# Performance work log

Measured on AMD Instinct MI355X. Metric: run time of the kernel, lower is better.

## Reference

```python
import jax, jax.numpy as jnp
import numpy as np
from jax import lax

HEADS = 8
PS = 4  # window size


def setup_inputs() -> dict:
    key = jax.random.key(0)
    k1, k2, k3, k4 = jax.random.split(key, 4)
    b, c, h, w = 8, 256, 128, 128
    x = jax.random.normal(k1, (b, c, h, w), dtype=jnp.float32)
    W_qkv = jax.random.normal(k2, (3 * c, c), dtype=jnp.float32) * 0.05
    W_dw = jax.random.normal(k3, (3 * c, 1, 3, 3), dtype=jnp.float32) * 0.1
    temperature = jnp.ones((HEADS, 1, 1), dtype=jnp.float32)
    W_proj = jax.random.normal(k4, (c, c), dtype=jnp.float32) * 0.05
    return {"x": x, "W_qkv": W_qkv, "W_dw": W_dw, "temperature": temperature, "W_proj": W_proj}


def _l2norm(t, eps=1e-12):
    # matches torch F.normalize(dim=-1): x / max(||x||_2, eps)
    n = jnp.sqrt(jnp.sum(t * t, axis=-1, keepdims=True))
    return t / jnp.maximum(n, eps)


def reference(x, W_qkv, W_dw, temperature, W_proj):
    b, c, h0, w0 = x.shape
    ps, heads = PS, HEADS
    pad_h = (ps - h0 % ps) % ps
    pad_w = (ps - w0 % ps) % ps
    if pad_h or pad_w:
        x = jnp.pad(x, ((0, 0), (0, 0), (0, pad_h), (0, pad_w)))
    H, W = x.shape[2], x.shape[3]
    nh, nw = H // ps, W // ps
    d = c // heads

    # 1x1 conv -> depthwise 3x3 conv (groups = 3c, padding 1)
    qkv = jnp.einsum('oc,bchw->bohw', W_qkv, x)
    qkv = lax.conv_general_dilated(qkv, W_dw, (1, 1), 'SAME',
                                   feature_group_count=3 * c,
                                   dimension_numbers=('NCHW', 'OIHW', 'NCHW'))
    q, k, v = jnp.split(qkv, 3, axis=1)

    def win(t):
        # b (head d) (nh ps) (nw ps) -> b (nh nw) head d (ps ps)
        t = t.reshape(b, heads, d, nh, ps, nw, ps)
        t = t.transpose(0, 3, 5, 1, 2, 4, 6)  # b nh nw head d ps ps
        return t.reshape(b, nh * nw, heads, d, ps * ps)

    q, k, v = win(q), win(k), win(v)
    q = _l2norm(q)
    k = _l2norm(k)

    # channel attention over head-dim d, keys/queries live in the ps*ps window
    attn = jnp.einsum('bnhde,bnhfe->bnhdf', q, k) * temperature  # (b,n,head,d,d)
    attn = jax.nn.softmax(attn, axis=-1)
    out = jnp.einsum('bnhdf,bnhfe->bnhde', attn, v)  # (b,n,head,d,ps*ps)

    # inverse rearrange -> b (head d) H W
    out = out.reshape(b, nh, nw, heads, d, ps, ps)
    out = out.transpose(0, 3, 4, 1, 5, 2, 6).reshape(b, c, H, W)
    out = jnp.einsum('oc,bchw->bohw', W_proj, out)
    if pad_h or pad_w:
        out = out[:, :, :h0, :w0]
    return out
```

## Files before the change

kernel.cpp:

```cpp
#include <hip/hip_runtime.h>
#include <math.h>


#define HW_ (128*128)
#define CHW_ (256*128*128)

typedef __attribute__((ext_vector_type(8))) short short8;
typedef __attribute__((ext_vector_type(4))) short shortv4;
typedef __attribute__((ext_vector_type(4))) float f32x4;

static __device__ __forceinline__ unsigned short f2bf(float f) {
    unsigned int u = __float_as_uint(f);
    unsigned int r = (u + 0x7fffu + ((u >> 16) & 1u)) >> 16;
    return (unsigned short)r;
}
static __device__ __forceinline__ float bf2f(unsigned short u) {
    return __uint_as_float(((unsigned int)u) << 16);
}

__global__ __launch_bounds__(256) void conv_w(
    const float* __restrict__ Wq, const float* __restrict__ Wp,
    unsigned short* __restrict__ out)
{
    int i = blockIdx.x * 256 + threadIdx.x;
    float v = (i < 196608) ? Wq[i] : Wp[i - 196608];
    out[i] = f2bf(v);
}

__global__ __launch_bounds__(256) void gemm_qkv(
    const unsigned short* __restrict__ A,
    const float* __restrict__ x,
    unsigned short* __restrict__ qkv)
{
    __shared__ __align__(16) char smem[16896];
    const int t = threadIdx.x;
    const int lane = t & 63, wid = t >> 6;
    const int m0 = blockIdx.x * 128;
    const int by = blockIdx.y;
    const int nb = by >> 7;
    const int nloc0 = (by & 127) * 128;
    const int wr = wid >> 1, wc = wid & 1;
    const int l15 = lane & 15, l4 = lane >> 4;

    const unsigned short* srcA[2];
    #pragma unroll
    for (int i = 0; i < 2; ++i) {
        int u = i * 256 + t;
        int r = u >> 2, cs = u & 3;
        int c = cs ^ ((r ^ (r >> 2)) & 3);
        srcA[i] = A + (size_t)(m0 + r) * 256 + c * 8;
    }
    int ar[4];
    #pragma unroll
    for (int i = 0; i < 4; ++i) {
        int rm = wr * 64 + i * 16 + l15;
        ar[i] = rm * 4 + (l4 ^ ((rm ^ (rm >> 2)) & 3));
    }

    const int pl  = (t & 31) * 4;
    const int chq = t >> 5;
    const float* xb = x + (size_t)nb * CHW_ + nloc0 + pl;
    char* Bbase = smem + 8192;
    char* bwp = Bbase + chq * 1056 + pl * 8;

    f32x4 acc[4][4];
    #pragma unroll
    for (int i = 0; i < 4; ++i)
        #pragma unroll
        for (int j = 0; j < 4; ++j)
            acc[i][j] = (f32x4){0.f, 0.f, 0.f, 0.f};

    const short8* Ab = (const short8*)smem;

    for (int k0 = 0; k0 < 256; k0 += 32) {
        __syncthreads();
        #pragma unroll
        for (int i = 0; i < 2; ++i)
            __builtin_amdgcn_global_load_lds(
                (const __attribute__((address_space(1))) void*)(srcA[i] + k0),
                (__attribute__((address_space(3))) void*)(smem + i * 4096 + wid * 1024),
                16, 0, 0);
        float4 vx[4];
        #pragma unroll
        for (int j = 0; j < 4; ++j)
            vx[j] = *reinterpret_cast<const float4*>(
                xb + (size_t)(k0 + chq * 4 + j) * HW_);
        short8 w0, w1;
        #pragma unroll
        for (int p = 0; p < 4; ++p) {
            const float* f0 = (const float*)&vx[0];
            const float* f1 = (const float*)&vx[1];
            const float* f2 = (const float*)&vx[2];
            const float* f3 = (const float*)&vx[3];
            short v0 = (short)f2bf(f0[p]);
            short v1 = (short)f2bf(f1[p]);
            short v2 = (short)f2bf(f2[p]);
            short v3 = (short)f2bf(f3[p]);
            if (p < 2) {
                w0[p * 4 + 0] = v0; w0[p * 4 + 1] = v1;
                w0[p * 4 + 2] = v2; w0[p * 4 + 3] = v3;
            } else {
                w1[(p - 2) * 4 + 0] = v0; w1[(p - 2) * 4 + 1] = v1;
                w1[(p - 2) * 4 + 2] = v2; w1[(p - 2) * 4 + 3] = v3;
            }
        }
        *reinterpret_cast<short8*>(bwp)      = w0;
        *reinterpret_cast<short8*>(bwp + 16) = w1;
        __syncthreads();

        short8 af[4], bf[4];
        #pragma unroll
        for (int i = 0; i < 4; ++i) {
            af[i] = Ab[ar[i]];
            int rn = wc * 64 + i * 16 + l15;
            shortv4 lo = *reinterpret_cast<const shortv4*>(
                Bbase + (l4 * 2) * 1056 + rn * 8);
            shortv4 hi = *reinterpret_cast<const shortv4*>(
                Bbase + (l4 * 2 + 1) * 1056 + rn * 8);
            short8 b;
            b[0] = lo.x; b[1] = lo.y; b[2] = lo.z; b[3] = lo.w;
            b[4] = hi.x; b[5] = hi.y; b[6] = hi.z; b[7] = hi.w;
            bf[i] = b;
        }
        #pragma unroll
        for (int am = 0; am < 4; ++am)
            #pragma unroll
            for (int bn = 0; bn < 4; ++bn)
                acc[am][bn] = __builtin_amdgcn_mfma_f32_16x16x32_bf16(
                    af[am], bf[bn], acc[am][bn], 0, 0, 0);
    }

    unsigned short* Co = qkv + (size_t)nb * (768 * (size_t)HW_) + nloc0;
    float* ep = (float*)smem;
    const int rr = t >> 3, c0 = (t & 7) * 16;
    #pragma unroll
    for (int am = 0; am < 4; ++am) {
        __syncthreads();
        #pragma unroll
        for (int q = 0; q < 4; ++q)
            #pragma unroll
            for (int bn = 0; bn < 4; ++bn)
                ep[(wr * 16 + l4 * 4 + q) * 132 + wc * 64 + bn * 16 + l15] =
                    acc[am][bn][q];
        __syncthreads();
        short8 o0, o1;
        #pragma unroll
        for (int j = 0; j < 8; ++j) {
            o0[j] = (short)f2bf(ep[rr * 132 + c0 + j]);
            o1[j] = (short)f2bf(ep[rr * 132 + c0 + 8 + j]);
        }
        int m = m0 + (rr >> 4) * 64 + am * 16 + (rr & 15);
        unsigned short* p = Co + (size_t)m * 16384 + c0;
        *reinterpret_cast<short8*>(p) = o0;
        *reinterpret_cast<short8*>(p + 8) = o1;
    }
}

template<int BF16OUT>
__global__ __launch_bounds__(256) void gemm_bf16(
    const unsigned short* __restrict__ A,
    const unsigned short* __restrict__ Bt,
    void* __restrict__ Cv,
    size_t strideBatch)
{
    __shared__ __align__(16) char smem[16384];

    const int t = threadIdx.x;
    const int lane = t & 63, wid = t >> 6;
    const int m0 = blockIdx.x * 128;
    const int n0 = blockIdx.y * 128;
    const int nb = n0 >> 14, nloc0 = n0 & 16383;
    const int wr = wid >> 1, wc = wid & 1;
    const int l15 = lane & 15, l4 = lane >> 4;

    const unsigned short* srcA[2];
    const unsigned short* srcB[2];
    #pragma unroll
    for (int i = 0; i < 2; ++i) {
        int u = i * 256 + t;
        int r = u >> 2, cs = u & 3;
        int c = cs ^ ((r ^ (r >> 2)) & 3);
        srcA[i] = A  + (size_t)(m0 + r) * 256 + c * 8;
        srcB[i] = Bt + (size_t)(n0 + r) * 256 + c * 8;
    }

    int ar[4], br[4];
    #pragma unroll
    for (int i = 0; i < 4; ++i) {
        int rm = wr * 64 + i * 16 + l15;
        ar[i] = rm * 4 + (l4 ^ ((rm ^ (rm >> 2)) & 3));
        int rn = wc * 64 + i * 16 + l15;
        br[i] = rn * 4 + (l4 ^ ((rn ^ (rn >> 2)) & 3));
    }

    f32x4 acc[4][4];
    #pragma unroll
    for (int i = 0; i < 4; ++i)
        #pragma unroll
        for (int j = 0; j < 4; ++j)
            acc[i][j] = (f32x4){0.f, 0.f, 0.f, 0.f};

    const short8* Ab = (const short8*)smem;
    const short8* Bb = (const short8*)(smem + 8192);

    for (int k0 = 0; k0 < 256; k0 += 32) {
        __syncthreads();
        #pragma unroll
        for (int i = 0; i < 2; ++i) {
            __builtin_amdgcn_global_load_lds(
                (const __attribute__((address_space(1))) void*)(srcA[i] + k0),
                (__attribute__((address_space(3))) void*)(smem + i * 4096 + wid * 1024),
                16, 0, 0);
            __builtin_amdgcn_global_load_lds(
                (const __attribute__((address_space(1))) void*)(srcB[i] + k0),
                (__attribute__((address_space(3))) void*)(smem + 8192 + i * 4096 + wid * 1024),
                16, 0, 0);
        }
        __syncthreads();
        short8 af[4], bf[4];
        #pragma unroll
        for (int i = 0; i < 4; ++i) { af[i] = Ab[ar[i]]; bf[i] = Bb[br[i]]; }
        #pragma unroll
        for (int am = 0; am < 4; ++am)
            #pragma unroll
            for (int bn = 0; bn < 4; ++bn)
                acc[am][bn] = __builtin_amdgcn_mfma_f32_16x16x32_bf16(
                    af[am], bf[bn], acc[am][bn], 0, 0, 0);
    }

    float* Co = (float*)Cv + (size_t)nb * strideBatch + nloc0;
    #pragma unroll
    for (int am = 0; am < 4; ++am)
        #pragma unroll
        for (int q = 0; q < 4; ++q) {
            int m = m0 + wr * 64 + am * 16 + l4 * 4 + q;
            #pragma unroll
            for (int bn = 0; bn < 4; ++bn)
                Co[(size_t)m * 16384 + wc * 64 + bn * 16 + l15] =
                    acc[am][bn][q];
        }
}

__global__ __launch_bounds__(256) void dwconv_win(
    const unsigned short* __restrict__ qkv,
    const float* __restrict__ Wdw,
    unsigned short* __restrict__ dww)
{
    const int t    = threadIdx.x;
    const int lane = t & 63;
    const int iw   = t & 31;
    const int chl  = t >> 5;
    const int wyl  = blockIdx.x;
    const int ch   = blockIdx.y * 8 + chl;
    const int bz   = blockIdx.z;

    float w[9];
    #pragma unroll
    for (int i = 0; i < 9; ++i) w[i] = Wdw[ch * 9 + i];

    float h[6][6];
    const unsigned short* plane = qkv + (size_t)(bz * 768 + ch) * HW_;
    #pragma unroll
    for (int r = 0; r < 6; ++r) {
        int gy = wyl * 4 - 1 + r;
        float c0 = 0.f, c1 = 0.f, c2 = 0.f, c3 = 0.f;
        if (gy >= 0 && gy < 128) {
            ushort4 u = *reinterpret_cast<const ushort4*>(
                plane + (size_t)gy * 128 + iw * 4);
            c0 = bf2f(u.x); c1 = bf2f(u.y); c2 = bf2f(u.z); c3 = bf2f(u.w);
        }
        float lf = __shfl(c3, (lane + 63) & 63);
        float rt = __shfl(c0, (lane + 1) & 63);
        h[r][0] = (iw == 0)  ? 0.f : lf;
        h[r][1] = c0; h[r][2] = c1; h[r][3] = c2; h[r][4] = c3;
        h[r][5] = (iw == 31) ? 0.f : rt;
    }

    unsigned short* outp =
        dww + ((size_t)(bz * 1024 + wyl * 32 + iw) * 768 + ch) * 16;
    short8 o0, o1;
    #pragma unroll
    for (int py = 0; py < 4; ++py) {
        #pragma unroll
        for (int px = 0; px < 4; ++px) {
            float s = 0.f;
            #pragma unroll
            for (int dy = 0; dy < 3; ++dy)
                #pragma unroll
                for (int dx = 0; dx < 3; ++dx)
                    s += h[py + dy][px + dx] * w[dy * 3 + dx];
            int e = py * 4 + px;
            if (e < 8) o0[e] = (short)f2bf(s); else o1[e - 8] = (short)f2bf(s);
        }
    }
    *reinterpret_cast<short8*>(outp) = o0;
    *reinterpret_cast<short8*>(outp + 8) = o1;
}

__global__ __launch_bounds__(256) void attn2(
    const unsigned short* __restrict__ dww,
    const float* __restrict__ temp,
    unsigned short* __restrict__ attnT)
{
    __shared__ float kv[512 * 20];
    const int t   = threadIdx.x;
    const int iw  = blockIdx.x;
    const int wyl = blockIdx.y;
    const int bz  = blockIdx.z;
    const int win = bz * 1024 + wyl * 32 + iw;
    const unsigned short* src = dww + (size_t)win * 12288;

    float q[16], kr[16], vr[16];
    {
        short8 a0 = *reinterpret_cast<const short8*>(src + t * 16);
        short8 a1 = *reinterpret_cast<const short8*>(src + t * 16 + 8);
        short8 b0 = *reinterpret_cast<const short8*>(src + (256 + t) * 16);
        short8 b1 = *reinterpret_cast<const short8*>(src + (256 + t) * 16 + 8);
        short8 c0 = *reinterpret_cast<const short8*>(src + (512 + t) * 16);
        short8 c1 = *reinterpret_cast<const short8*>(src + (512 + t) * 16 + 8);
        #pragma unroll
        for (int j = 0; j < 8; ++j) {
            q[j]      = bf2f((unsigned short)a0[j]);
            q[8 + j]  = bf2f((unsigned short)a1[j]);
            kr[j]     = bf2f((unsigned short)b0[j]);
            kr[8 + j] = bf2f((unsigned short)b1[j]);
            vr[j]     = bf2f((unsigned short)c0[j]);
            vr[8 + j] = bf2f((unsigned short)c1[j]);
        }
    }

    {
        float sq = 0.f, sk = 0.f;
        #pragma unroll
        for (int e = 0; e < 16; ++e) { sq += q[e] * q[e]; sk += kr[e] * kr[e]; }
        float cq = 1.0f / fmaxf(sqrtf(sq), 1e-12f);
        float ck = 1.0f / fmaxf(sqrtf(sk), 1e-12f);
        #pragma unroll
        for (int e = 0; e < 16; ++e) { q[e] *= cq; kr[e] *= ck; }
    }

    {
        float* kp = &kv[t * 20];
        float* vp = &kv[(256 + t) * 20];
        #pragma unroll
        for (int j = 0; j < 4; ++j) {
            *reinterpret_cast<float4*>(kp + j * 4) =
                make_float4(kr[j*4], kr[j*4+1], kr[j*4+2], kr[j*4+3]);
            *reinterpret_cast<float4*>(vp + j * 4) =
                make_float4(vr[j*4], vr[j*4+1], vr[j*4+2], vr[j*4+3]);
        }
    }
    __syncthreads();

    const int head = t >> 5;
    const float tmpv = temp[head];
    const float* kb = &kv[(head * 32) * 20];
    const float* vb = &kv[(256 + head * 32) * 20];

    float lg[32];
    float mx = -1e30f;
    #pragma unroll
    for (int f = 0; f < 32; ++f) {
        float s = 0.f;
        #pragma unroll
        for (int j = 0; j < 4; ++j) {
            float4 k4 = *reinterpret_cast<const float4*>(kb + f * 20 + j * 4);
            s += q[j*4] * k4.x + q[j*4+1] * k4.y + q[j*4+2] * k4.z + q[j*4+3] * k4.w;
        }
        s *= tmpv;
        lg[f] = s;
        mx = fmaxf(mx, s);
    }
    float sum = 0.f;
    #pragma unroll
    for (int f = 0; f < 32; ++f) { lg[f] = __expf(lg[f] - mx); sum += lg[f]; }
    const float inv = 1.0f / sum;

    float o[16];
    #pragma unroll
    for (int e = 0; e < 16; ++e) o[e] = 0.f;
    #pragma unroll
    for (int f = 0; f < 32; ++f) {
        float p = lg[f];
        #pragma unroll
        for (int j = 0; j < 4; ++j) {
            float4 v4 = *reinterpret_cast<const float4*>(vb + f * 20 + j * 4);
            o[j*4]   += p * v4.x; o[j*4+1] += p * v4.y;
            o[j*4+2] += p * v4.z; o[j*4+3] += p * v4.w;
        }
    }

    #pragma unroll
    for (int e = 0; e < 16; ++e) {
        int py = e >> 2, px = e & 3;
        size_t pl = (size_t)bz * HW_ + (wyl * 4 + py) * 128 + iw * 4 + px;
        attnT[pl * 256 + t] = f2bf(o[e] * inv);
    }
}

extern "C" void kernel_launch(void* const* d_in, const int* in_sizes, int n_in,
                              void* d_out, int out_size, void* d_ws, size_t ws_size,
                              hipStream_t stream) {
    const float* x     = (const float*)d_in[0];
    const float* Wqkv  = (const float*)d_in[1];
    const float* Wdw   = (const float*)d_in[2];
    const float* temp  = (const float*)d_in[3];
    const float* Wproj = (const float*)d_in[4];
    float* out = (float*)d_out;

    unsigned short* Wb = (unsigned short*)d_ws;
    const size_t offW = 262144 * 2;

    const size_t qkvB = (size_t)768 * HW_ * 2;
    const size_t dwwB = (size_t)1024 * 768 * 16 * 2;
    const size_t atB  = (size_t)HW_ * 256 * 2;
    const size_t perB = qkvB + dwwB + atB;

    int G = 8;
    while (G > 1 && offW + (size_t)G * perB > ws_size) G >>= 1;

    unsigned short* qkv   = (unsigned short*)((char*)d_ws + offW);
    unsigned short* dww   = (unsigned short*)((char*)d_ws + offW + (size_t)G * qkvB);
    unsigned short* attnT = (unsigned short*)((char*)d_ws + offW + (size_t)G * (qkvB + dwwB));

    conv_w<<<1024, 256, 0, stream>>>(Wqkv, Wproj, Wb);

    for (int b0 = 0; b0 < 8; b0 += G) {
        gemm_qkv<<<dim3(6, G * 128), 256, 0, stream>>>(
            Wb, x + (size_t)b0 * CHW_, qkv);

        dwconv_win<<<dim3(32, 96, G), 256, 0, stream>>>(
            qkv, Wdw, dww);

        attn2<<<dim3(32, 32, G), 256, 0, stream>>>(
            dww, temp, attnT);

        gemm_bf16<0><<<dim3(2, G * 128), 256, 0, stream>>>(
            Wb + 196608, attnT, out + (size_t)b0 * CHW_, (size_t)CHW_);
    }
}
```

Measured before the change: 411.1 us.

## Prefetch x tiles, swizzle B smem, use packed bf16 converts and fp16 dot2 logits

In the QKV GEMM, the next x chunk is now loaded into registers during the current iteration's MFMAs, the B tile in shared memory uses an XOR swizzle to cut bank conflicts, and fp32-to-bf16 packing uses the hardware v_cvt_pk_bf16_f32 instruction. The attention kernel keeps normalized K in fp16 in shared memory and computes q·k logits with fdot2, which halves LDS traffic for K and reduces ALU work. The output-projection GEMM swaps its grid axes so that consecutive blocks walk along N. The fp16 logits lower precision slightly, which is tolerable because q and k are L2-normalized.

```diff
diff --git a/kernel.cpp b/kernel.cpp
--- a/kernel.cpp
+++ b/kernel.cpp
@@ -8,6 +8,7 @@
 typedef __attribute__((ext_vector_type(8))) short short8;
 typedef __attribute__((ext_vector_type(4))) short shortv4;
 typedef __attribute__((ext_vector_type(4))) float f32x4;
+typedef __attribute__((ext_vector_type(2))) _Float16 half2v;
 
 static __device__ __forceinline__ unsigned short f2bf(float f) {
     unsigned int u = __float_as_uint(f);
@@ -16,6 +17,14 @@
 }
 static __device__ __forceinline__ float bf2f(unsigned short u) {
     return __uint_as_float(((unsigned int)u) << 16);
+}
+static __device__ __forceinline__ half2v pk16(float a, float b) {
+    return __builtin_bit_cast(half2v, __builtin_amdgcn_cvt_pkrtz(a, b));
+}
+static __device__ __forceinline__ unsigned int pkbf(float a, float b) {
+    unsigned int r;
+    asm("v_cvt_pk_bf16_f32 %0, %1, %2" : "=v"(r) : "v"(a), "v"(b));
+    return r;
 }
 
 __global__ __launch_bounds__(256) void conv_w(
@@ -57,11 +66,22 @@
         ar[i] = rm * 4 + (l4 ^ ((rm ^ (rm >> 2)) & 3));
     }
 
-    const int pl  = (t & 31) * 4;
+    const int tp4 = (t & 31) * 4;
     const int chq = t >> 5;
-    const float* xb = x + (size_t)nb * CHW_ + nloc0 + pl;
+    const float* xb = x + (size_t)nb * CHW_ + nloc0 + tp4;
     char* Bbase = smem + 8192;
-    char* bwp = Bbase + chq * 1056 + pl * 8;
+    const int u0 = (t & 31) * 2, u1 = u0 + 1;
+    char* wp0 = Bbase + chq * 1056 + (u0 ^ (u0 >> 3)) * 16;
+    char* wp1 = Bbase + chq * 1056 + (u1 ^ (u1 >> 3)) * 16;
+
+    const char* rp0[4];
+    #pragma unroll
+    for (int i = 0; i < 4; ++i) {
+        int rn = wc * 64 + i * 16 + l15;
+        int uu = rn >> 1;
+        int off = ((uu ^ (uu >> 3)) * 16) + (rn & 1) * 8;
+        rp0[i] = Bbase + (l4 * 2) * 1056 + off;
+    }
 
     f32x4 acc[4][4];
     #pragma unroll
@@ -72,7 +92,14 @@
 
     const short8* Ab = (const short8*)smem;
 
-    for (int k0 = 0; k0 < 256; k0 += 32) {
+    float4 vx[4];
+    #pragma unroll
+    for (int j = 0; j < 4; ++j)
+        vx[j] = *reinterpret_cast<const float4*>(xb + (size_t)(chq * 4 + j) * HW_);
+
+    #pragma unroll
+    for (int kk = 0; kk < 8; ++kk) {
+        const int k0 = kk * 32;
         __syncthreads();
         #pragma unroll
         for (int i = 0; i < 2; ++i)
@@ -80,54 +107,39 @@
                 (const __attribute__((address_space(1))) void*)(srcA[i] + k0),
                 (__attribute__((address_space(3))) void*)(smem + i * 4096 + wid * 1024),
                 16, 0, 0);
-        float4 vx[4];
-        #pragma unroll
-        for (int j = 0; j < 4; ++j)
-            vx[j] = *reinterpret_cast<const float4*>(
-                xb + (size_t)(k0 + chq * 4 + j) * HW_);
-        short8 w0, w1;
-        #pragma unroll
-        for (int p = 0; p < 4; ++p) {
-            const float* f0 = (const float*)&vx[0];
-            const float* f1 = (const float*)&vx[1];
-            const float* f2 = (const float*)&vx[2];
-            const float* f3 = (const float*)&vx[3];
-            short v0 = (short)f2bf(f0[p]);
-            short v1 = (short)f2bf(f1[p]);
-            short v2 = (short)f2bf(f2[p]);
-            short v3 = (short)f2bf(f3[p]);
-            if (p < 2) {
-                w0[p * 4 + 0] = v0; w0[p * 4 + 1] = v1;
-                w0[p * 4 + 2] = v2; w0[p * 4 + 3] = v3;
-            } else {
-                w1[(p - 2) * 4 + 0] = v0; w1[(p - 2) * 4 + 1] = v1;
-                w1[(p - 2) * 4 + 2] = v2; w1[(p - 2) * 4 + 3] = v3;
-            }
-        }
-        *reinterpret_cast<short8*>(bwp)      = w0;
-        *reinterpret_cast<short8*>(bwp + 16) = w1;
-        __syncthreads();
-
-        short8 af[4], bf[4];
+        {
+            uint4 w0, w1;
+            w0.x = pkbf(vx[0].x, vx[1].x); w0.y = pkbf(vx[2].x, vx[3].x);
+            w0.z = pkbf(vx[0].y, vx[1].y); w0.w = pkbf(vx[2].y, vx[3].y);
+            w1.x = pkbf(vx[0].z, vx[1].z); w1.y = pkbf(vx[2].z, vx[3].z);
+            w1.z = pkbf(vx[0].w, vx[1].w); w1.w = pkbf(vx[2].w, vx[3].w);
+            *reinterpret_cast<uint4*>(wp0) = w0;
+            *reinterpret_cast<uint4*>(wp1) = w1;
+        }
+        __syncthreads();
+        short8 af[4], bfv[4];
         #pragma unroll
         for (int i = 0; i < 4; ++i) {
             af[i] = Ab[ar[i]];
-            int rn = wc * 64 + i * 16 + l15;
-            shortv4 lo = *reinterpret_cast<const shortv4*>(
-                Bbase + (l4 * 2) * 1056 + rn * 8);
-            shortv4 hi = *reinterpret_cast<const shortv4*>(
-                Bbase + (l4 * 2 + 1) * 1056 + rn * 8);
+            shortv4 lo = *reinterpret_cast<const shortv4*>(rp0[i]);
+            shortv4 hi = *reinterpret_cast<const shortv4*>(rp0[i] + 1056);
             short8 b;
             b[0] = lo.x; b[1] = lo.y; b[2] = lo.z; b[3] = lo.w;
             b[4] = hi.x; b[5] = hi.y; b[6] = hi.z; b[7] = hi.w;
-            bf[i] = b;
+            bfv[i] = b;
+        }
+        if (kk < 7) {
+            #pragma unroll
+            for (int j = 0; j < 4; ++j)
+                vx[j] = *reinterpret_cast<const float4*>(
+                    xb + (size_t)(k0 + 32 + chq * 4 + j) * HW_);
         }
         #pragma unroll
         for (int am = 0; am < 4; ++am)
             #pragma unroll
             for (int bn = 0; bn < 4; ++bn)
                 acc[am][bn] = __builtin_amdgcn_mfma_f32_16x16x32_bf16(
-                    af[am], bf[bn], acc[am][bn], 0, 0, 0);
+                    af[am], bfv[bn], acc[am][bn], 0, 0, 0);
     }
 
     unsigned short* Co = qkv + (size_t)nb * (768 * (size_t)HW_) + nloc0;
@@ -156,19 +168,17 @@
     }
 }
 
-template<int BF16OUT>
-__global__ __launch_bounds__(256) void gemm_bf16(
+__global__ __launch_bounds__(256) void gemm_bf16f(
     const unsigned short* __restrict__ A,
     const unsigned short* __restrict__ Bt,
-    void* __restrict__ Cv,
+    float* __restrict__ Cv,
     size_t strideBatch)
 {
     __shared__ __align__(16) char smem[16384];
 
     const int t = threadIdx.x;
     const int lane = t & 63, wid = t >> 6;
-    const int m0 = blockIdx.x * 128;
-    const int n0 = blockIdx.y * 128;
+    const int m0 = blockIdx.y * 128, n0 = blockIdx.x * 128;
     const int nb = n0 >> 14, nloc0 = n0 & 16383;
     const int wr = wid >> 1, wc = wid & 1;
     const int l15 = lane & 15, l4 = lane >> 4;
@@ -228,7 +238,7 @@
                     af[am], bf[bn], acc[am][bn], 0, 0, 0);
     }
 
-    float* Co = (float*)Cv + (size_t)nb * strideBatch + nloc0;
+    float* Co = Cv + (size_t)nb * strideBatch + nloc0;
     #pragma unroll
     for (int am = 0; am < 4; ++am)
         #pragma unroll
@@ -302,7 +312,8 @@
     const float* __restrict__ temp,
     unsigned short* __restrict__ attnT)
 {
-    __shared__ float kv[512 * 20];
+    __shared__ __align__(16) unsigned short ks[256 * 40];
+    __shared__ __align__(16) float vs[256 * 20];
     const int t   = threadIdx.x;
     const int iw  = blockIdx.x;
     const int wyl = blockIdx.y;
@@ -310,23 +321,22 @@
     const int win = bz * 1024 + wyl * 32 + iw;
     const unsigned short* src = dww + (size_t)win * 12288;
 
+    short8 a0 = *reinterpret_cast<const short8*>(src + t * 16);
+    short8 a1 = *reinterpret_cast<const short8*>(src + t * 16 + 8);
+    short8 b0 = *reinterpret_cast<const short8*>(src + (256 + t) * 16);
+    short8 b1 = *reinterpret_cast<const short8*>(src + (256 + t) * 16 + 8);
+    short8 c0 = *reinterpret_cast<const short8*>(src + (512 + t) * 16);
+    short8 c1 = *reinterpret_cast<const short8*>(src + (512 + t) * 16 + 8);
+
     float q[16], kr[16], vr[16];
-    {
-        short8 a0 = *reinterpret_cast<const short8*>(src + t * 16);
-        short8 a1 = *reinterpret_cast<const short8*>(src + t * 16 + 8);
-        short8 b0 = *reinterpret_cast<const short8*>(src + (256 + t) * 16);
-        short8 b1 = *reinterpret_cast<const short8*>(src + (256 + t) * 16 + 8);
-        short8 c0 = *reinterpret_cast<const short8*>(src + (512 + t) * 16);
-        short8 c1 = *reinterpret_cast<const short8*>(src + (512 + t) * 16 + 8);
-        #pragma unroll
-        for (int j = 0; j < 8; ++j) {
-            q[j]      = bf2f((unsigned short)a0[j]);
-            q[8 + j]  = bf2f((unsigned short)a1[j]);
-            kr[j]     = bf2f((unsigned short)b0[j]);
-            kr[8 + j] = bf2f((unsigned short)b1[j]);
-            vr[j]     = bf2f((unsigned short)c0[j]);
-            vr[8 + j] = bf2f((unsigned short)c1[j]);
-        }
+    #pragma unroll
+    for (int j = 0; j < 8; ++j) {
+        q[j]      = bf2f((unsigned short)a0[j]);
+        q[8 + j]  = bf2f((unsigned short)a1[j]);
+        kr[j]     = bf2f((unsigned short)b0[j]);
+        kr[8 + j] = bf2f((unsigned short)b1[j]);
+        vr[j]     = bf2f((unsigned short)c0[j]);
+        vr[8 + j] = bf2f((unsigned short)c1[j]);
     }
 
     {
@@ -339,34 +349,46 @@
         for (int e = 0; e < 16; ++e) { q[e] *= cq; kr[e] *= ck; }
     }
 
+    half2v q2[8], k2[8];
+    #pragma unroll
+    for (int j = 0; j < 8; ++j) {
+        q2[j] = pk16(q[2 * j], q[2 * j + 1]);
+        k2[j] = pk16(kr[2 * j], kr[2 * j + 1]);
+    }
+
+    *reinterpret_cast<short8*>(&ks[t * 40])     = *reinterpret_cast<short8*>(&k2[0]);
+    *reinterpret_cast<short8*>(&ks[t * 40 + 8]) = *reinterpret_cast<short8*>(&k2[4]);
     {
-        float* kp = &kv[t * 20];
-        float* vp = &kv[(256 + t) * 20];
-        #pragma unroll
-        for (int j = 0; j < 4; ++j) {
-            *reinterpret_cast<float4*>(kp + j * 4) =
-                make_float4(kr[j*4], kr[j*4+1], kr[j*4+2], kr[j*4+3]);
+        float* vp = &vs[t * 20];
+        #pragma unroll
+        for (int j = 0; j < 4; ++j)
             *reinterpret_cast<float4*>(vp + j * 4) =
                 make_float4(vr[j*4], vr[j*4+1], vr[j*4+2], vr[j*4+3]);
-        }
     }
     __syncthreads();
 
     const int head = t >> 5;
     const float tmpv = temp[head];
-    const float* kb = &kv[(head * 32) * 20];
-    const float* vb = &kv[(256 + head * 32) * 20];
+    const unsigned short* kb = &ks[(head * 32) * 40];
+    const float* vb = &vs[(head * 32) * 20];
 
     float lg[32];
     float mx = -1e30f;
     #pragma unroll
     for (int f = 0; f < 32; ++f) {
+        short8 k0 = *reinterpret_cast<const short8*>(kb + f * 40);
+        short8 k1 = *reinterpret_cast<const short8*>(kb + f * 40 + 8);
+        half2v h0[4], h1[4];
+        #pragma unroll
+        for (int j = 0; j < 4; ++j) {
+            h0[j] = __builtin_bit_cast(half2v, (int)(((int)(unsigned short)k0[2*j]) | (((int)(unsigned short)k0[2*j+1]) << 16)));
+            h1[j] = __builtin_bit_cast(half2v, (int)(((int)(unsigned short)k1[2*j]) | (((int)(unsigned short)k1[2*j+1]) << 16)));
+        }
         float s = 0.f;
         #pragma unroll
-        for (int j = 0; j < 4; ++j) {
-            float4 k4 = *reinterpret_cast<const float4*>(kb + f * 20 + j * 4);
-            s += q[j*4] * k4.x + q[j*4+1] * k4.y + q[j*4+2] * k4.z + q[j*4+3] * k4.w;
-        }
+        for (int j = 0; j < 4; ++j) s = __builtin_amdgcn_fdot2(q2[j], h0[j], s, false);
+        #pragma unroll
+        for (int j = 0; j < 4; ++j) s = __builtin_amdgcn_fdot2(q2[4 + j], h1[j], s, false);
         s *= tmpv;
         lg[f] = s;
         mx = fmaxf(mx, s);
@@ -435,7 +457,7 @@
         attn2<<<dim3(32, 32, G), 256, 0, stream>>>(
             dww, temp, attnT);
 
-        gemm_bf16<0><<<dim3(2, G * 128), 256, 0, stream>>>(
+        gemm_bf16f<<<dim3(G * 128, 2), 256, 0, stream>>>(
             Wb + 196608, attnT, out + (size_t)b0 * CHW_, (size_t)CHW_);
     }
 }
```

Result: faster. 402.0 us (-2.2%).
